# Optimization experiments

Measured on AMD Instinct MI355X. Metric: run time of the kernel, lower is better.

## Reference

```python
import jax, jax.numpy as jnp
import numpy as np

CODEBOOK_SIZE = 8192
EMBED_DIM = 128
BETA = 0.25
TEMPERATURE = 0.1
EPS_NORM = 1e-12  # torch F.normalize eps


def _l2_normalize(x, axis=-1):
    n = jnp.linalg.norm(x, axis=axis, keepdims=True)
    return x / jnp.maximum(n, EPS_NORM)


def setup_inputs() -> dict:
    key = jax.random.key(0)
    kz, kw = jax.random.split(key)
    z = jax.random.normal(kz, (4, 4096, EMBED_DIM), dtype=jnp.float32)
    # torch init is uniform(-1/D, 1/D); normal also exercises the math fine,
    # but stay faithful to scale:
    W = jax.random.uniform(kw, (CODEBOOK_SIZE, EMBED_DIM), dtype=jnp.float32,
                           minval=-1.0 / EMBED_DIM, maxval=1.0 / EMBED_DIM)
    return {"z": z, "W": W}


def reference(z, W):
    orig_shape = z.shape
    z_flat = z.reshape(-1, EMBED_DIM)              # [N, D]
    N = z_flat.shape[0]

    z_norm = _l2_normalize(z_flat, axis=1)
    e_norm = _l2_normalize(W, axis=1)
    scores = z_norm @ e_norm.T                     # [N, K]

    idx = jnp.argmax(scores, axis=1)               # [N]
    z_q = W[idx].reshape(orig_shape)

    counts = jnp.zeros((CODEBOOK_SIZE,), jnp.float32).at[idx].add(1.0)
    e_mean = counts / N
    perplexity = jnp.exp(-jnp.sum(e_mean * jnp.log(e_mean + 1e-8)))

    sg = jax.lax.stop_gradient
    commit_loss = jnp.mean((sg(z_q) - z) ** 2) + BETA * jnp.mean((z_q - sg(z)) ** 2)

    z_q_st = z + sg(z_q - z)                        # straight-through

    log_probs = jax.nn.log_softmax(scores / TEMPERATURE, axis=1)  # [N, K]
    probs = jnp.exp(log_probs)
    P_avg = jnp.mean(probs, axis=0) + 1e-8
    entropy_loss = -jnp.sum(P_avg * jnp.log(P_avg))

    return (z_q_st, commit_loss, perplexity, entropy_loss)
```

## Files before the change

kernel.cpp:

```cpp
#include <hip/hip_runtime.h>
#include <hip/hip_bf16.h>
#include <math.h>

#define N_ROWS 16384
#define DIM 128
#define K_CODES 8192
#define EPS2 2e-3f
#define EPSF 7e-5f

#define OFF_EN       0u
#define OFF_ZN       1048576u
#define OFF_EP       3145728u
#define OFF_ZP       4194304u
#define OFF_ZC       6291456u
#define OFF_PART     7340032u
#define OFF_PART2    7602176u
#define OFF_LINV     7864320u
#define OFF_IDX      7880704u
#define OFF_FLA      7897088u
#define OFF_FLB      7913472u
#define OFF_CNT      7929856u
#define OFF_P        7938048u
#define OFF_MSE      7946240u
#define OFF_NFA      7946241u
#define OFF_NFB      7946242u
#define OFF_REFBUF   7946244u
#define MEMSET_BYTES 196624u

typedef __bf16 bf16x8 __attribute__((ext_vector_type(8)));
typedef float  f32x4  __attribute__((ext_vector_type(4)));
#define MFMA16(a, b, c) __builtin_amdgcn_mfma_f32_16x16x32_bf16(a, b, c, 0, 0, 0)

__device__ __forceinline__ void gld_lds16(const ushort* g, ushort* l) {
    __builtin_amdgcn_global_load_lds(
        (const __attribute__((address_space(1))) unsigned int*)g,
        (__attribute__((address_space(3))) unsigned int*)l, 16, 0, 0);
}

__device__ __forceinline__ ushort f2bf(float x) {
    __hip_bfloat16 b = __float2bfloat16(x);
    return *reinterpret_cast<ushort*>(&b);
}
__device__ __forceinline__ float bf2f(ushort u) {
    __hip_bfloat16 b = *reinterpret_cast<__hip_bfloat16*>(&u);
    return __bfloat162float(b);
}

__device__ __forceinline__ void bf_store2(ushort* __restrict__ P, int T, int r,
                                          int rx, int k, ushort e0, ushort e1) {
    int g = k >> 6, kp = (k >> 3) & 7, j = k & 7;
    int off = (((((T << 2) + g) << 10) + (r << 3) + (kp ^ rx)) << 3) + j;
    *reinterpret_cast<ushort2*>(&P[off]) = make_ushort2(e0, e1);
}

__global__ __launch_bounds__(256) void k_prep(const float* __restrict__ z,
                                              const float* __restrict__ W,
                                              float* __restrict__ zN,
                                              float* __restrict__ eN,
                                              ushort* __restrict__ Zp,
                                              ushort* __restrict__ Ep) {
    int t = threadIdx.x, w = t >> 6, lane = t & 63;
    int row = blockIdx.x * 4 + w;
    const float* src; float* dstN; ushort* dstP;
    if (row < N_ROWS) { src = z; dstN = zN; dstP = Zp; }
    else { row -= N_ROWS; src = W; dstN = eN; dstP = Ep; }
    float2 v = *reinterpret_cast<const float2*>(&src[(size_t)row * DIM + lane * 2]);
    float ss = v.x * v.x + v.y * v.y;
#pragma unroll
    for (int off = 32; off; off >>= 1) ss += __shfl_xor(ss, off);
    float nrm = fmaxf(sqrtf(ss), 1e-12f);
    float a = v.x / nrm, b = v.y / nrm;
    *reinterpret_cast<float2*>(&dstN[(size_t)row * DIM + lane * 2]) = make_float2(a, b);
    ushort ha = f2bf(a), hb = f2bf(b);
    ushort la = f2bf(a - bf2f(ha)), lb = f2bf(b - bf2f(hb));
    int T = row >> 7, r = row & 127, rx = r & 7, d = lane * 2;
    bf_store2(dstP, T, r, rx, d, ha, hb);
    bf_store2(dstP, T, r, rx, 128 + d, la, lb);
}

__global__ __launch_bounds__(256, 2) void k_p1(const ushort* __restrict__ Zp,
                                               const ushort* __restrict__ Ep,
                                               float4* __restrict__ part) {
    __shared__ ushort Bu[2][16384];
    int t = threadIdx.x, lane = t & 63, w = t >> 6;
    int rg = blockIdx.x >> 2, slice = blockIdx.x & 3;
    int wm = w >> 1, wn = w & 1;
    int n15 = lane & 15, quad = lane >> 4;
    int T = rg >> 1, rofs = (rg & 1) << 6;

    bf16x8 af[2][2][2];
#pragma unroll
    for (int ms = 0; ms < 2; ++ms) {
        int r = rofs + wm * 32 + ms * 16 + n15, rx = r & 7;
#pragma unroll
        for (int g = 0; g < 2; ++g)
#pragma unroll
            for (int kl = 0; kl < 2; ++kl)
                af[ms][g][kl] = *reinterpret_cast<const bf16x8*>(
                    &Zp[(((((T << 2) + g) << 10) + (r << 3) + (((kl * 4 + quad)) ^ rx)) << 3)]);
    }

    float sm[8], s2v[8], sl[8];
    unsigned si[8];
#pragma unroll
    for (int s = 0; s < 8; ++s) { sm[s] = -1e30f; s2v[s] = -1e30f; sl[s] = 0.f; si[s] = 0u; }

    {
        const ushort* gb = Ep + (((size_t)(slice * 16) << 2) << 13);
#pragma unroll
        for (int it = 0; it < 8; ++it) {
            int cpos = it * 256 + t;
            gld_lds16(gb + (cpos << 3), &Bu[0][cpos << 3]);
        }
    }
    int bufc = 0;
    for (int ch = 0; ch < 16; ++ch) {
        __syncthreads();
        if (ch < 15) {
            const ushort* gb = Ep + (((size_t)((slice * 16 + ch + 1) << 2)) << 13);
            ushort* dst = Bu[bufc ^ 1];
#pragma unroll
            for (int it = 0; it < 8; ++it) {
                int cpos = it * 256 + t;
                gld_lds16(gb + (cpos << 3), &dst[cpos << 3]);
            }
        }
        const ushort* bsrc = Bu[bufc];
        f32x4 acc[2][4];
#pragma unroll
        for (int i = 0; i < 2; ++i)
#pragma unroll
            for (int j = 0; j < 4; ++j) acc[i][j] = (f32x4)2.0f;
#pragma unroll
        for (int g = 0; g < 2; ++g)
#pragma unroll
            for (int kl = 0; kl < 2; ++kl) {
                bf16x8 bfr[4];
#pragma unroll
                for (int ns = 0; ns < 4; ++ns) {
                    int c = wn * 64 + ns * 16 + n15;
                    int kx = (kl * 4 + quad) ^ (c & 7);
                    bfr[ns] = *reinterpret_cast<const bf16x8*>(
                        &bsrc[(((g << 10) + (c << 3) + kx) << 3)]);
                }
#pragma unroll
                for (int ms = 0; ms < 2; ++ms)
#pragma unroll
                    for (int ns = 0; ns < 4; ++ns)
                        acc[ms][ns] = MFMA16(af[ms][g][kl], bfr[ns], acc[ms][ns]);
            }
        unsigned cbase = (unsigned)((slice * 16 + ch) * 128 + wn * 64 + n15);
#pragma unroll
        for (int ms = 0; ms < 2; ++ms)
#pragma unroll
            for (int reg = 0; reg < 4; ++reg) {
                int s = ms * 4 + reg;
                float m = sm[s], m2 = s2v[s], l = 0.f;
                unsigned idx = si[s];
#pragma unroll
                for (int ns = 0; ns < 4; ++ns) {
                    float v = acc[ms][ns][reg];
                    l += __expf(fmaf(v, 10.f, -20.f));
                    float lo = fminf(v, m);
                    m2 = fmaxf(m2, lo);
                    idx = (v > m) ? (cbase + ns * 16) : idx;
                    m = fmaxf(v, m);
                }
                sl[s] += l; sm[s] = m; s2v[s] = m2; si[s] = idx;
            }
        bufc ^= 1;
    }
#pragma unroll
    for (int ms = 0; ms < 2; ++ms)
#pragma unroll
        for (int reg = 0; reg < 4; ++reg) {
            int s = ms * 4 + reg;
            float m = sm[s], m2 = s2v[s], l = sl[s];
            unsigned idx = si[s];
#pragma unroll
            for (int off = 1; off < 16; off <<= 1) {
                float om  = __shfl_xor(m, off);
                float om2 = __shfl_xor(m2, off);
                float ol  = __shfl_xor(l, off);
                unsigned oi = (unsigned)__shfl_xor((int)idx, off);
                m2 = fmaxf(fmaxf(m2, om2), fminf(m, om));
                l += ol;
                bool take = (om > m) || (om == m && oi < idx);
                idx = take ? oi : idx;
                m = fmaxf(m, om);
            }
            if (n15 == 0) {
                int row = rg * 64 + wm * 32 + ms * 16 + quad * 4 + reg;
                part[slice * N_ROWS + row] = make_float4(m, l, __uint_as_float(idx), m2);
            }
        }
}

__global__ __launch_bounds__(256) void k_merge(const float4* __restrict__ part,
                                               float* __restrict__ linv_out,
                                               int* __restrict__ idx_out,
                                               unsigned int* __restrict__ counts,
                                               int* __restrict__ flaglistA,
                                               int* __restrict__ nfA) {
    int row = blockIdx.x * 256 + threadIdx.x;
    float m = -1e30f, m2 = -1e30f, l = 0.f;
    unsigned idx = 0u;
#pragma unroll
    for (int s = 0; s < 4; ++s) {
        float4 p = part[s * N_ROWS + row];
        float om = p.x, ol = p.y, om2 = p.w;
        unsigned oi = __float_as_uint(p.z);
        m2 = fmaxf(fmaxf(m2, om2), fminf(m, om));
        l += ol;
        bool take = (om > m) || (om == m && oi < idx);
        idx = take ? oi : idx;
        m = fmaxf(m, om);
    }
    linv_out[row] = 1.0f / l;
    idx_out[row] = (int)idx;
    atomicAdd(&counts[idx], 1u);
    if (m - m2 < EPS2) {
        int pos = atomicAdd(nfA, 1);
        if (pos < 8192) flaglistA[pos] = row;
    }
}

__global__ __launch_bounds__(256) void k_gather2(const ushort* __restrict__ Zp,
                                                 const int* __restrict__ flaglistA,
                                                 const int* __restrict__ nfA,
                                                 ushort* __restrict__ Zc) {
    int nf2 = *nfA; if (nf2 > 8192) nf2 = 8192;
    int total = nf2 * 32;
    const uint4* srcv = reinterpret_cast<const uint4*>(Zp);
    uint4* dstv = reinterpret_cast<uint4*>(Zc);
    for (int c = blockIdx.x * 256 + threadIdx.x; c < total; c += 65536) {
        int crow = c >> 5, g = (c >> 3) & 3, kp = c & 7;
        int row = flaglistA[crow];
        int Ts = row >> 7, rs = row & 127;
        int sidx = (((Ts << 2) + g) << 10) + (rs << 3) + (kp ^ (rs & 7));
        int Td = crow >> 6, rd = crow & 63;
        int didx = (((Td << 2) + g) << 9) + (rd << 3) + (kp ^ (rd & 7));
        dstv[didx] = srcv[sidx];
    }
}

__global__ __launch_bounds__(256, 2) void k_s2(const ushort* __restrict__ Zc,
                                               const ushort* __restrict__ Ep,
                                               const int* __restrict__ nfA,
                                               float4* __restrict__ part2) {
    __shared__ ushort Bu[2][8192];
    int nf2 = *nfA; if (nf2 > 8192) nf2 = 8192;
    int cg2 = blockIdx.x >> 3, csl = blockIdx.x & 7;
    if (cg2 * 64 >= nf2) return;
    int t = threadIdx.x, lane = t & 63, w = t >> 6;
    int wm = w >> 1, wn = w & 1;
    int n15 = lane & 15, quad = lane >> 4;

    bf16x8 af[2][4][2];
#pragma unroll
    for (int ms = 0; ms < 2; ++ms) {
        int r = wm * 32 + ms * 16 + n15, rx = r & 7;
#pragma unroll
        for (int gz = 0; gz < 4; ++gz)
#pragma unroll
            for (int kl = 0; kl < 2; ++kl)
                af[ms][gz][kl] = *reinterpret_cast<const bf16x8*>(
                    &Zc[(((((cg2 << 2) + gz) << 9) + (r << 3) + ((kl * 4 + quad) ^ rx)) << 3)]);
    }

    float sm[8], s2v[8];
    unsigned si[8];
#pragma unroll
    for (int s = 0; s < 8; ++s) { sm[s] = -1e30f; s2v[s] = -1e30f; si[s] = 0u; }

    {
        const ushort* gb = Ep + (((size_t)((csl * 8) << 2)) << 13);
#pragma unroll
        for (int it = 0; it < 4; ++it) {
            int cpos = it * 256 + t;
            gld_lds16(gb + (cpos << 3), &Bu[0][cpos << 3]);
        }
    }
    int bufc = 0;
    f32x4 acc[2][4];
#pragma unroll
    for (int i = 0; i < 2; ++i)
#pragma unroll
        for (int j = 0; j < 4; ++j) acc[i][j] = (f32x4)2.0f;

    for (int st = 0; st < 32; ++st) {
        __syncthreads();
        if (st < 31) {
            int nx = st + 1;
            const ushort* gb = Ep + (((size_t)(((csl * 8 + (nx >> 2)) << 2) + (nx & 3))) << 13);
            ushort* dst = Bu[bufc ^ 1];
#pragma unroll
            for (int it = 0; it < 4; ++it) {
                int cpos = it * 256 + t;
                gld_lds16(gb + (cpos << 3), &dst[cpos << 3]);
            }
        }
        const ushort* bsrc = Bu[bufc];
        int ge = st & 3;
        int a0 = ge & 1, a1 = (ge & 1) + 2;
        bool two = (ge < 2);
#pragma unroll
        for (int kl = 0; kl < 2; ++kl) {
            bf16x8 bfr[4];
#pragma unroll
            for (int ns = 0; ns < 4; ++ns) {
                int c = wn * 64 + ns * 16 + n15;
                int kx = (kl * 4 + quad) ^ (c & 7);
                bfr[ns] = *reinterpret_cast<const bf16x8*>(&bsrc[(((c << 3) + kx) << 3)]);
            }
#pragma unroll
            for (int ms = 0; ms < 2; ++ms)
#pragma unroll
                for (int ns = 0; ns < 4; ++ns)
                    acc[ms][ns] = MFMA16(af[ms][a0][kl], bfr[ns], acc[ms][ns]);
            if (two) {
#pragma unroll
                for (int ms = 0; ms < 2; ++ms)
#pragma unroll
                    for (int ns = 0; ns < 4; ++ns)
                        acc[ms][ns] = MFMA16(af[ms][a1][kl], bfr[ns], acc[ms][ns]);
            }
        }
        if (ge == 3) {
            int ch = st >> 2;
            unsigned cbase = (unsigned)((csl * 8 + ch) * 128 + wn * 64 + n15);
#pragma unroll
            for (int ms = 0; ms < 2; ++ms)
#pragma unroll
                for (int reg = 0; reg < 4; ++reg) {
                    int s = ms * 4 + reg;
                    float m = sm[s], m2 = s2v[s];
                    unsigned idx = si[s];
#pragma unroll
                    for (int ns = 0; ns < 4; ++ns) {
                        float v = acc[ms][ns][reg];
                        float lo = fminf(v, m);
                        m2 = fmaxf(m2, lo);
                        idx = (v > m) ? (cbase + ns * 16) : idx;
                        m = fmaxf(v, m);
                    }
                    sm[s] = m; s2v[s] = m2; si[s] = idx;
                }
#pragma unroll
            for (int i = 0; i < 2; ++i)
#pragma unroll
                for (int j = 0; j < 4; ++j) acc[i][j] = (f32x4)2.0f;
        }
        bufc ^= 1;
    }
#pragma unroll
    for (int ms = 0; ms < 2; ++ms)
#pragma unroll
        for (int reg = 0; reg < 4; ++reg) {
            int s = ms * 4 + reg;
            float m = sm[s], m2 = s2v[s];
            unsigned idx = si[s];
#pragma unroll
            for (int off = 1; off < 16; off <<= 1) {
                float om  = __shfl_xor(m, off);
                float om2 = __shfl_xor(m2, off);
                unsigned oi = (unsigned)__shfl_xor((int)idx, off);
                m2 = fmaxf(fmaxf(m2, om2), fminf(m, om));
                bool take = (om > m) || (om == m && oi < idx);
                idx = take ? oi : idx;
                m = fmaxf(m, om);
            }
            if (n15 == 0) {
                int crow = cg2 * 64 + wm * 32 + ms * 16 + quad * 4 + reg;
                part2[csl * 8192 + crow] = make_float4(m, 0.f, __uint_as_float(idx), m2);
            }
        }
}

__global__ __launch_bounds__(256) void k_merge2(const float4* __restrict__ part2,
                                                const int* __restrict__ flaglistA,
                                                const int* __restrict__ nfA,
                                                int* __restrict__ idx_arr,
                                                unsigned int* __restrict__ counts,
                                                int* __restrict__ flaglistB,
                                                int* __restrict__ nfB) {
    int i = blockIdx.x * 256 + threadIdx.x;
    int nf2 = *nfA; if (nf2 > 8192) nf2 = 8192;
    if (i >= nf2) return;
    int row = flaglistA[i];
    float m = -1e30f, m2 = -1e30f;
    unsigned idx = 0u;
#pragma unroll
    for (int s = 0; s < 8; ++s) {
        float4 p = part2[s * 8192 + i];
        float om = p.x, om2 = p.w;
        unsigned oi = __float_as_uint(p.z);
        m2 = fmaxf(fmaxf(m2, om2), fminf(m, om));
        bool take = (om > m) || (om == m && oi < idx);
        idx = take ? oi : idx;
        m = fmaxf(m, om);
    }
    int newi = (int)idx, oldi = idx_arr[row];
    if (newi != oldi) {
        idx_arr[row] = newi;
        atomicAdd(&counts[oldi], 0xFFFFFFFFu);
        atomicAdd(&counts[newi], 1u);
    }
    if (m - m2 < EPSF) {
        int pos = atomicAdd(nfB, 1);
        if (pos < N_ROWS) flaglistB[pos] = row;
    }
}

__global__ __launch_bounds__(256) void k_refine(const float* __restrict__ zN,
                                                const float* __restrict__ eN,
                                                const int* __restrict__ flaglistB,
                                                const int* __restrict__ nfB,
                                                unsigned long long* __restrict__ refbuf) {
    int nf = *nfB;
    if (nf > N_ROWS) nf = N_ROWS;
    int csl = blockIdx.x & 7;
    int t = threadIdx.x;
    __shared__ float zl[DIM];
    for (int fi = blockIdx.x >> 3; fi < nf; fi += 512) {
        int row = flaglistB[fi];
        __syncthreads();
        if (t < DIM) zl[t] = zN[(size_t)row * DIM + t];
        __syncthreads();
        double best = -1e300;
        int bc = 0x7FFFFFFF;
#pragma unroll
        for (int j = 0; j < 4; ++j) {
            int c = csl * 1024 + j * 256 + t;
            const float* e = &eN[(size_t)c * DIM];
            double s = 0.0;
#pragma unroll 8
            for (int d = 0; d < DIM; ++d) s += (double)zl[d] * (double)e[d];
            if (s > best) { best = s; bc = c; }
        }
#pragma unroll
        for (int off = 1; off < 64; off <<= 1) {
            double ob = __shfl_xor(best, off);
            int oc = __shfl_xor(bc, off);
            if (ob > best || (ob == best && oc < bc)) { best = ob; bc = oc; }
        }
        if ((t & 63) == 0) {
            unsigned long long u = (unsigned long long)__double_as_longlong(best);
            u = (u & 0x8000000000000000ull) ? ~u : (u | 0x8000000000000000ull);
            unsigned long long key = (u & ~0x1FFFull) | (unsigned long long)(8191 - bc);
            atomicMax(&refbuf[row], key);
        }
    }
}

__global__ __launch_bounds__(256) void k_fixidx(const int* __restrict__ flaglistB,
                                                const int* __restrict__ nfB,
                                                const unsigned long long* __restrict__ refbuf,
                                                int* __restrict__ idx,
                                                unsigned int* __restrict__ counts) {
    int i = blockIdx.x * 256 + threadIdx.x;
    int nf = *nfB;
    if (nf > N_ROWS) nf = N_ROWS;
    if (i < nf) {
        int row = flaglistB[i];
        int newi = 8191 - (int)(refbuf[row] & 0x1FFFull);
        int oldi = idx[row];
        if (newi != oldi) {
            idx[row] = newi;
            atomicAdd(&counts[oldi], 0xFFFFFFFFu);
            atomicAdd(&counts[newi], 1u);
        }
    }
}

__global__ __launch_bounds__(256, 2) void k_p2(const ushort* __restrict__ Zp,
                                               const ushort* __restrict__ Ep,
                                               const float* __restrict__ linv_in,
                                               float* __restrict__ P_sum) {
    __shared__ ushort Bu[2][16384];
    int t = threadIdx.x, lane = t & 63, w = t >> 6;
    int cg = blockIdx.x >> 2, rslice = blockIdx.x & 3;
    int wm = w >> 1, wn = w & 1;
    int n15 = lane & 15, quad = lane >> 4;
    int T = cg >> 1, cofs = (cg & 1) << 6;

    bf16x8 af[2][2][2];
#pragma unroll
    for (int ms = 0; ms < 2; ++ms) {
        int c = cofs + wm * 32 + ms * 16 + n15, cx = c & 7;
#pragma unroll
        for (int g = 0; g < 2; ++g)
#pragma unroll
            for (int kl = 0; kl < 2; ++kl)
                af[ms][g][kl] = *reinterpret_cast<const bf16x8*>(
                    &Ep[(((((T << 2) + g) << 10) + (c << 3) + ((kl * 4 + quad) ^ cx)) << 3)]);
    }

    float pacc[8];
#pragma unroll
    for (int s = 0; s < 8; ++s) pacc[s] = 0.f;

    {
        const ushort* gb = Zp + (((size_t)((rslice * 32) << 2)) << 13);
#pragma unroll
        for (int it = 0; it < 8; ++it) {
            int cpos = it * 256 + t;
            gld_lds16(gb + (cpos << 3), &Bu[0][cpos << 3]);
        }
    }
    int bufc = 0;
    for (int ch = 0; ch < 32; ++ch) {
        __syncthreads();
        if (ch < 31) {
            const ushort* gb = Zp + (((size_t)((rslice * 32 + ch + 1) << 2)) << 13);
            ushort* dst = Bu[bufc ^ 1];
#pragma unroll
            for (int it = 0; it < 8; ++it) {
                int cpos = it * 256 + t;
                gld_lds16(gb + (cpos << 3), &dst[cpos << 3]);
            }
        }
        const ushort* bsrc = Bu[bufc];
        f32x4 acc[2][4];
#pragma unroll
        for (int i = 0; i < 2; ++i)
#pragma unroll
            for (int j = 0; j < 4; ++j) acc[i][j] = (f32x4)2.0f;
#pragma unroll
        for (int g = 0; g < 2; ++g)
#pragma unroll
            for (int kl = 0; kl < 2; ++kl) {
                bf16x8 bfr[4];
#pragma unroll
                for (int ns = 0; ns < 4; ++ns) {
                    int r = wn * 64 + ns * 16 + n15;
                    int kx = (kl * 4 + quad) ^ (r & 7);
                    bfr[ns] = *reinterpret_cast<const bf16x8*>(
                        &bsrc[(((g << 10) + (r << 3) + kx) << 3)]);
                }
#pragma unroll
                for (int ms = 0; ms < 2; ++ms)
#pragma unroll
                    for (int ns = 0; ns < 4; ++ns)
                        acc[ms][ns] = MFMA16(af[ms][g][kl], bfr[ns], acc[ms][ns]);
            }
        int rbase = (rslice * 32 + ch) * 128 + wn * 64 + n15;
        float li[4];
#pragma unroll
        for (int ns = 0; ns < 4; ++ns) li[ns] = linv_in[rbase + ns * 16];
#pragma unroll
        for (int ms = 0; ms < 2; ++ms)
#pragma unroll
            for (int reg = 0; reg < 4; ++reg) {
                int s = ms * 4 + reg;
                float p = pacc[s];
#pragma unroll
                for (int ns = 0; ns < 4; ++ns)
                    p = fmaf(__expf(fmaf(acc[ms][ns][reg], 10.f, -20.f)), li[ns], p);
                pacc[s] = p;
            }
        bufc ^= 1;
    }
#pragma unroll
    for (int s = 0; s < 8; ++s) {
#pragma unroll
        for (int off = 1; off < 16; off <<= 1) pacc[s] += __shfl_xor(pacc[s], off);
    }
    if (n15 == 0) {
#pragma unroll
        for (int ms = 0; ms < 2; ++ms)
#pragma unroll
            for (int reg = 0; reg < 4; ++reg)
                atomicAdd(&P_sum[cg * 64 + wm * 32 + ms * 16 + quad * 4 + reg],
                          pacc[ms * 4 + reg]);
    }
}

__global__ __launch_bounds__(256) void k_gather(const float* __restrict__ z,
                                                const float* __restrict__ W,
                                                const int* __restrict__ idx,
                                                float* __restrict__ out,
                                                float* __restrict__ mse) {
    int v = blockIdx.x * 256 + threadIdx.x;
    int row = v >> 5;
    int id = idx[row];
    float4 q = *reinterpret_cast<const float4*>(&W[(size_t)id * DIM + (v & 31) * 4]);
    float4 zz = *reinterpret_cast<const float4*>(&z[(size_t)v * 4]);
    float dx = q.x - zz.x, dy = q.y - zz.y, dz = q.z - zz.z, dw = q.w - zz.w;
    *reinterpret_cast<float4*>(&out[(size_t)v * 4]) = q;
    float e = dx * dx + dy * dy + dz * dz + dw * dw;
#pragma unroll
    for (int off = 1; off < 64; off <<= 1) e += __shfl_xor(e, off);
    __shared__ float red[4];
    int lane = threadIdx.x & 63, wv = threadIdx.x >> 6;
    if (lane == 0) red[wv] = e;
    __syncthreads();
    if (threadIdx.x == 0) atomicAdd(mse, red[0] + red[1] + red[2] + red[3]);
}

__global__ __launch_bounds__(256) void k_finalize(const unsigned int* __restrict__ counts,
                                                  const float* __restrict__ P_sum,
                                                  const float* __restrict__ mse,
                                                  float* __restrict__ out) {
    int t = threadIdx.x;
    float s1 = 0.f, s2 = 0.f;
    for (int k = t; k < K_CODES; k += 256) {
        float em = (float)counts[k] * (1.0f / 16384.0f);
        s1 += em * logf(em + 1e-8f);
        float p = P_sum[k] * (1.0f / 16384.0f) + 1e-8f;
        s2 += p * logf(p);
    }
#pragma unroll
    for (int off = 1; off < 64; off <<= 1) {
        s1 += __shfl_xor(s1, off);
        s2 += __shfl_xor(s2, off);
    }
    __shared__ float r1[4], r2[4];
    int lane = t & 63, wv = t >> 6;
    if (lane == 0) { r1[wv] = s1; r2[wv] = s2; }
    __syncthreads();
    if (t == 0) {
        float S1 = r1[0] + r1[1] + r1[2] + r1[3];
        float S2 = r2[0] + r2[1] + r2[2] + r2[3];
        out[2097152] = 1.25f * mse[0] * (1.0f / 2097152.0f);
        out[2097153] = expf(-S1);
        out[2097154] = -S2;
    }
}

extern "C" void kernel_launch(void* const* d_in, const int* in_sizes, int n_in,
                              void* d_out, int out_size, void* d_ws, size_t ws_size,
                              hipStream_t stream) {
    (void)in_sizes; (void)n_in; (void)out_size; (void)ws_size;
    const float* z = (const float*)d_in[0];
    const float* W = (const float*)d_in[1];
    float* ws = (float*)d_ws;
    float* eN = ws + OFF_EN;
    float* zN = ws + OFF_ZN;
    ushort* Ep = (ushort*)(ws + OFF_EP);
    ushort* Zp = (ushort*)(ws + OFF_ZP);
    ushort* Zc = (ushort*)(ws + OFF_ZC);
    float4* part = (float4*)(ws + OFF_PART);
    float4* part2 = (float4*)(ws + OFF_PART2);
    float* linv = ws + OFF_LINV;
    int* idx = (int*)(ws + OFF_IDX);
    int* flaglistA = (int*)(ws + OFF_FLA);
    int* flaglistB = (int*)(ws + OFF_FLB);
    unsigned int* counts = (unsigned int*)(ws + OFF_CNT);
    float* P = ws + OFF_P;
    float* mse = ws + OFF_MSE;
    int* nfA = (int*)(ws + OFF_NFA);
    int* nfB = (int*)(ws + OFF_NFB);
    unsigned long long* refbuf = (unsigned long long*)(ws + OFF_REFBUF);
    float* out = (float*)d_out;

    hipMemsetAsync(ws + OFF_CNT, 0, MEMSET_BYTES, stream);
    k_prep<<<(N_ROWS + K_CODES) / 4, 256, 0, stream>>>(z, W, zN, eN, Zp, Ep);
    k_p1<<<1024, 256, 0, stream>>>(Zp, Ep, part);
    k_merge<<<N_ROWS / 256, 256, 0, stream>>>(part, linv, idx, counts, flaglistA, nfA);
    k_gather2<<<256, 256, 0, stream>>>(Zp, flaglistA, nfA, Zc);
    k_s2<<<1024, 256, 0, stream>>>(Zc, Ep, nfA, part2);
    k_merge2<<<32, 256, 0, stream>>>(part2, flaglistA, nfA, idx, counts, flaglistB, nfB);
    k_refine<<<4096, 256, 0, stream>>>(zN, eN, flaglistB, nfB, refbuf);
    k_fixidx<<<64, 256, 0, stream>>>(flaglistB, nfB, refbuf, idx, counts);
    k_p2<<<512, 256, 0, stream>>>(Zp, Ep, linv, P);
    k_gather<<<(N_ROWS * DIM / 4) / 256, 256, 0, stream>>>(z, W, idx, out, mse);
    k_finalize<<<1, 256, 0, stream>>>(counts, P, mse, out);
}
```

Before: 309.7 us.

## Halve LDS staging tiles, raise occupancy, pack argmax index into score bits

k_p1 and k_p2 now stage 64-column half tiles, so the LDS double buffer is half as large and launch bounds rise to 4 blocks per SM. k_p2 also doubles its grid by splitting the row slices. k_p1 encodes the candidate index in the low 6 mantissa bits of each score, so the running max carries the index and the separate index registers and selects go away. Exponentials use exp2 with pre-scaled constants. The hipMemsetAsync is replaced by zeroing inside k_prep, saving one launch. The mantissa packing slightly perturbs score values, so near-ties may resolve differently, and the smaller tiles double the number of barriers.

```diff
diff --git a/kernel.cpp b/kernel.cpp
--- a/kernel.cpp
+++ b/kernel.cpp
@@ -25,11 +25,22 @@
 #define OFF_NFA      7946241u
 #define OFF_NFB      7946242u
 #define OFF_REFBUF   7946244u
-#define MEMSET_BYTES 196624u
+#define ZERO_WORDS   49156u
 
 typedef __bf16 bf16x8 __attribute__((ext_vector_type(8)));
 typedef float  f32x4  __attribute__((ext_vector_type(4)));
 #define MFMA16(a, b, c) __builtin_amdgcn_mfma_f32_16x16x32_bf16(a, b, c, 0, 0, 0)
+
+#if defined(__has_builtin)
+#if __has_builtin(__builtin_amdgcn_exp2f)
+#define EXP2F(x) __builtin_amdgcn_exp2f(x)
+#endif
+#endif
+#ifndef EXP2F
+#define EXP2F(x) exp2f(x)
+#endif
+#define L2E10 14.4269504089f
+#define L2E10B 28.8539008178f
 
 __device__ __forceinline__ void gld_lds16(const ushort* g, ushort* l) {
     __builtin_amdgcn_global_load_lds(
@@ -53,13 +64,29 @@
     *reinterpret_cast<ushort2*>(&P[off]) = make_ushort2(e0, e1);
 }
 
+__device__ __forceinline__ void stage64(const ushort* __restrict__ src, int Tc, int h,
+                                        ushort* __restrict__ dst, int t) {
+#pragma unroll
+    for (int it = 0; it < 4; ++it) {
+        int i = it * 256 + t;
+        int g = i >> 9, within = i & 511;
+        int schunk = (((Tc << 2) + g) << 10) + (h << 9) + within;
+        gld_lds16(src + ((size_t)schunk << 3), dst + ((size_t)((g << 9) + within) << 3));
+    }
+}
+
 __global__ __launch_bounds__(256) void k_prep(const float* __restrict__ z,
                                               const float* __restrict__ W,
                                               float* __restrict__ zN,
                                               float* __restrict__ eN,
                                               ushort* __restrict__ Zp,
-                                              ushort* __restrict__ Ep) {
+                                              ushort* __restrict__ Ep,
+                                              unsigned* __restrict__ zr) {
     int t = threadIdx.x, w = t >> 6, lane = t & 63;
+    if (blockIdx.x < 193) {
+        unsigned i = blockIdx.x * 256 + t;
+        if (i < ZERO_WORDS) zr[i] = 0u;
+    }
     int row = blockIdx.x * 4 + w;
     const float* src; float* dstN; ushort* dstP;
     if (row < N_ROWS) { src = z; dstN = zN; dstP = Zp; }
@@ -78,10 +105,10 @@
     bf_store2(dstP, T, r, rx, 128 + d, la, lb);
 }
 
-__global__ __launch_bounds__(256, 2) void k_p1(const ushort* __restrict__ Zp,
+__global__ __launch_bounds__(256, 4) void k_p1(const ushort* __restrict__ Zp,
                                                const ushort* __restrict__ Ep,
                                                float4* __restrict__ part) {
-    __shared__ ushort Bu[2][16384];
+    __shared__ ushort Bu[2][8192];
     int t = threadIdx.x, lane = t & 63, w = t >> 6;
     int rg = blockIdx.x >> 2, slice = blockIdx.x & 3;
     int wm = w >> 1, wn = w & 1;
@@ -97,77 +124,79 @@
 #pragma unroll
             for (int kl = 0; kl < 2; ++kl)
                 af[ms][g][kl] = *reinterpret_cast<const bf16x8*>(
-                    &Zp[(((((T << 2) + g) << 10) + (r << 3) + (((kl * 4 + quad)) ^ rx)) << 3)]);
+                    &Zp[(((((T << 2) + g) << 10) + (r << 3) + ((kl * 4 + quad) ^ rx)) << 3)]);
     }
 
     float sm[8], s2v[8], sl[8];
-    unsigned si[8];
-#pragma unroll
-    for (int s = 0; s < 8; ++s) { sm[s] = -1e30f; s2v[s] = -1e30f; sl[s] = 0.f; si[s] = 0u; }
-
-    {
-        const ushort* gb = Ep + (((size_t)(slice * 16) << 2) << 13);
-#pragma unroll
-        for (int it = 0; it < 8; ++it) {
-            int cpos = it * 256 + t;
-            gld_lds16(gb + (cpos << 3), &Bu[0][cpos << 3]);
-        }
-    }
+#pragma unroll
+    for (int s = 0; s < 8; ++s) { sm[s] = -1e30f; s2v[s] = -1e30f; sl[s] = 0.f; }
+
+    stage64(Ep, slice * 16, 0, Bu[0], t);
     int bufc = 0;
-    for (int ch = 0; ch < 16; ++ch) {
+    f32x4 acc[2][4];
+#pragma unroll
+    for (int i = 0; i < 2; ++i)
+#pragma unroll
+        for (int j = 0; j < 4; ++j) acc[i][j] = (f32x4)2.0f;
+
+    for (int st = 0; st < 32; ++st) {
         __syncthreads();
-        if (ch < 15) {
-            const ushort* gb = Ep + (((size_t)((slice * 16 + ch + 1) << 2)) << 13);
-            ushort* dst = Bu[bufc ^ 1];
-#pragma unroll
-            for (int it = 0; it < 8; ++it) {
-                int cpos = it * 256 + t;
-                gld_lds16(gb + (cpos << 3), &dst[cpos << 3]);
-            }
+        if (st < 31) {
+            int nx = st + 1;
+            stage64(Ep, slice * 16 + (nx >> 1), nx & 1, Bu[bufc ^ 1], t);
         }
         const ushort* bsrc = Bu[bufc];
-        f32x4 acc[2][4];
-#pragma unroll
-        for (int i = 0; i < 2; ++i)
-#pragma unroll
-            for (int j = 0; j < 4; ++j) acc[i][j] = (f32x4)2.0f;
+        int sp = st & 1;
 #pragma unroll
         for (int g = 0; g < 2; ++g)
 #pragma unroll
             for (int kl = 0; kl < 2; ++kl) {
-                bf16x8 bfr[4];
-#pragma unroll
-                for (int ns = 0; ns < 4; ++ns) {
-                    int c = wn * 64 + ns * 16 + n15;
+                bf16x8 bfr[2];
+#pragma unroll
+                for (int nsl = 0; nsl < 2; ++nsl) {
+                    int c = wn * 32 + nsl * 16 + n15;
                     int kx = (kl * 4 + quad) ^ (c & 7);
-                    bfr[ns] = *reinterpret_cast<const bf16x8*>(
-                        &bsrc[(((g << 10) + (c << 3) + kx) << 3)]);
+                    bfr[nsl] = *reinterpret_cast<const bf16x8*>(
+                        &bsrc[((size_t)((g << 9) + (c << 3) + kx)) << 3]);
                 }
 #pragma unroll
                 for (int ms = 0; ms < 2; ++ms)
 #pragma unroll
-                    for (int ns = 0; ns < 4; ++ns)
-                        acc[ms][ns] = MFMA16(af[ms][g][kl], bfr[ns], acc[ms][ns]);
-            }
-        unsigned cbase = (unsigned)((slice * 16 + ch) * 128 + wn * 64 + n15);
-#pragma unroll
-        for (int ms = 0; ms < 2; ++ms)
-#pragma unroll
-            for (int reg = 0; reg < 4; ++reg) {
-                int s = ms * 4 + reg;
-                float m = sm[s], m2 = s2v[s], l = 0.f;
-                unsigned idx = si[s];
-#pragma unroll
-                for (int ns = 0; ns < 4; ++ns) {
-                    float v = acc[ms][ns][reg];
-                    l += __expf(fmaf(v, 10.f, -20.f));
-                    float lo = fminf(v, m);
-                    m2 = fmaxf(m2, lo);
-                    idx = (v > m) ? (cbase + ns * 16) : idx;
-                    m = fmaxf(v, m);
+                    for (int nsl = 0; nsl < 2; ++nsl)
+                        acc[ms][sp * 2 + nsl] = MFMA16(af[ms][g][kl], bfr[nsl], acc[ms][sp * 2 + nsl]);
+            }
+        if (sp) {
+            int pair = st >> 1;
+            unsigned base6 = 63u - (unsigned)(pair * 4);
+#pragma unroll
+            for (int ms = 0; ms < 2; ++ms)
+#pragma unroll
+                for (int reg = 0; reg < 4; ++reg) {
+                    int s = ms * 4 + reg;
+                    float v0 = acc[ms][0][reg], v1 = acc[ms][1][reg];
+                    float v2 = acc[ms][2][reg], v3 = acc[ms][3][reg];
+                    float e0 = EXP2F(fmaf(v0, L2E10, -L2E10B));
+                    float e1 = EXP2F(fmaf(v1, L2E10, -L2E10B));
+                    float e2 = EXP2F(fmaf(v2, L2E10, -L2E10B));
+                    float e3 = EXP2F(fmaf(v3, L2E10, -L2E10B));
+                    sl[s] += (e0 + e1) + (e2 + e3);
+                    float f0 = __uint_as_float((__float_as_uint(v0) & 0xFFFFFFC0u) | (base6 - 0u));
+                    float f1 = __uint_as_float((__float_as_uint(v1) & 0xFFFFFFC0u) | (base6 - 1u));
+                    float f2 = __uint_as_float((__float_as_uint(v2) & 0xFFFFFFC0u) | (base6 - 2u));
+                    float f3 = __uint_as_float((__float_as_uint(v3) & 0xFFFFFFC0u) | (base6 - 3u));
+                    float a  = fmaxf(f0, f1), b = fminf(f0, f1);
+                    float c2 = fmaxf(f2, f3), d = fminf(f2, f3);
+                    float chmax = fmaxf(a, c2);
+                    float sec4 = fmaxf(fmaxf(fminf(a, c2), b), d);
+                    float mo = sm[s];
+                    s2v[s] = fmaxf(fmaxf(s2v[s], fminf(mo, chmax)), sec4);
+                    sm[s] = fmaxf(mo, chmax);
                 }
-                sl[s] += l; sm[s] = m; s2v[s] = m2; si[s] = idx;
-            }
+#pragma unroll
+            for (int i = 0; i < 2; ++i)
+#pragma unroll
+                for (int j = 0; j < 4; ++j) acc[i][j] = (f32x4)2.0f;
+        }
         bufc ^= 1;
     }
 #pragma unroll
@@ -176,7 +205,10 @@
         for (int reg = 0; reg < 4; ++reg) {
             int s = ms * 4 + reg;
             float m = sm[s], m2 = s2v[s], l = sl[s];
-            unsigned idx = si[s];
+            unsigned c6 = 63u - (__float_as_uint(m) & 63u);
+            int pair = (int)(c6 >> 2), j = (int)(c6 & 3u);
+            unsigned idx = (unsigned)(slice * 2048 + pair * 128 + wn * 32 +
+                                      (j >> 1) * 64 + (j & 1) * 16 + n15);
 #pragma unroll
             for (int off = 1; off < 16; off <<= 1) {
                 float om  = __shfl_xor(m, off);
@@ -473,13 +505,13 @@
     }
 }
 
-__global__ __launch_bounds__(256, 2) void k_p2(const ushort* __restrict__ Zp,
+__global__ __launch_bounds__(256, 4) void k_p2(const ushort* __restrict__ Zp,
                                                const ushort* __restrict__ Ep,
                                                const float* __restrict__ linv_in,
                                                float* __restrict__ P_sum) {
-    __shared__ ushort Bu[2][16384];
+    __shared__ ushort Bu[2][8192];
     int t = threadIdx.x, lane = t & 63, w = t >> 6;
-    int cg = blockIdx.x >> 2, rslice = blockIdx.x & 3;
+    int cg = blockIdx.x >> 3, rslice = blockIdx.x & 7;
     int wm = w >> 1, wn = w & 1;
     int n15 = lane & 15, quad = lane >> 4;
     int T = cg >> 1, cofs = (cg & 1) << 6;
@@ -500,63 +532,48 @@
 #pragma unroll
     for (int s = 0; s < 8; ++s) pacc[s] = 0.f;
 
-    {
-        const ushort* gb = Zp + (((size_t)((rslice * 32) << 2)) << 13);
-#pragma unroll
-        for (int it = 0; it < 8; ++it) {
-            int cpos = it * 256 + t;
-            gld_lds16(gb + (cpos << 3), &Bu[0][cpos << 3]);
-        }
-    }
+    stage64(Zp, rslice * 16, 0, Bu[0], t);
     int bufc = 0;
-    for (int ch = 0; ch < 32; ++ch) {
+    for (int st = 0; st < 32; ++st) {
         __syncthreads();
-        if (ch < 31) {
-            const ushort* gb = Zp + (((size_t)((rslice * 32 + ch + 1) << 2)) << 13);
-            ushort* dst = Bu[bufc ^ 1];
-#pragma unroll
-            for (int it = 0; it < 8; ++it) {
-                int cpos = it * 256 + t;
-                gld_lds16(gb + (cpos << 3), &dst[cpos << 3]);
-            }
+        if (st < 31) {
+            int nx = st + 1;
+            stage64(Zp, rslice * 16 + (nx >> 1), nx & 1, Bu[bufc ^ 1], t);
         }
         const ushort* bsrc = Bu[bufc];
-        f32x4 acc[2][4];
+        f32x4 acc[2][2];
 #pragma unroll
         for (int i = 0; i < 2; ++i)
 #pragma unroll
-            for (int j = 0; j < 4; ++j) acc[i][j] = (f32x4)2.0f;
+            for (int j = 0; j < 2; ++j) acc[i][j] = (f32x4)2.0f;
 #pragma unroll
         for (int g = 0; g < 2; ++g)
 #pragma unroll
             for (int kl = 0; kl < 2; ++kl) {
-                bf16x8 bfr[4];
-#pragma unroll
-                for (int ns = 0; ns < 4; ++ns) {
-                    int r = wn * 64 + ns * 16 + n15;
+                bf16x8 bfr[2];
+#pragma unroll
+                for (int nsl = 0; nsl < 2; ++nsl) {
+                    int r = wn * 32 + nsl * 16 + n15;
                     int kx = (kl * 4 + quad) ^ (r & 7);
-                    bfr[ns] = *reinterpret_cast<const bf16x8*>(
-                        &bsrc[(((g << 10) + (r << 3) + kx) << 3)]);
+                    bfr[nsl] = *reinterpret_cast<const bf16x8*>(
+                        &bsrc[((size_t)((g << 9) + (r << 3) + kx)) << 3]);
                 }
 #pragma unroll
                 for (int ms = 0; ms < 2; ++ms)
 #pragma unroll
-                    for (int ns = 0; ns < 4; ++ns)
-                        acc[ms][ns] = MFMA16(af[ms][g][kl], bfr[ns], acc[ms][ns]);
-            }
-        int rbase = (rslice * 32 + ch) * 128 + wn * 64 + n15;
-        float li[4];
-#pragma unroll
-        for (int ns = 0; ns < 4; ++ns) li[ns] = linv_in[rbase + ns * 16];
+                    for (int nsl = 0; nsl < 2; ++nsl)
+                        acc[ms][nsl] = MFMA16(af[ms][g][kl], bfr[nsl], acc[ms][nsl]);
+            }
+        int rbase = rslice * 2048 + st * 64 + wn * 32 + n15;
+        float li0 = linv_in[rbase], li1 = linv_in[rbase + 16];
 #pragma unroll
         for (int ms = 0; ms < 2; ++ms)
 #pragma unroll
             for (int reg = 0; reg < 4; ++reg) {
                 int s = ms * 4 + reg;
                 float p = pacc[s];
-#pragma unroll
-                for (int ns = 0; ns < 4; ++ns)
-                    p = fmaf(__expf(fmaf(acc[ms][ns][reg], 10.f, -20.f)), li[ns], p);
+                p = fmaf(EXP2F(fmaf(acc[ms][0][reg], L2E10, -L2E10B)), li0, p);
+                p = fmaf(EXP2F(fmaf(acc[ms][1][reg], L2E10, -L2E10B)), li1, p);
                 pacc[s] = p;
             }
         bufc ^= 1;
@@ -654,8 +671,7 @@
     unsigned long long* refbuf = (unsigned long long*)(ws + OFF_REFBUF);
     float* out = (float*)d_out;
 
-    hipMemsetAsync(ws + OFF_CNT, 0, MEMSET_BYTES, stream);
-    k_prep<<<(N_ROWS + K_CODES) / 4, 256, 0, stream>>>(z, W, zN, eN, Zp, Ep);
+    k_prep<<<(N_ROWS + K_CODES) / 4, 256, 0, stream>>>(z, W, zN, eN, Zp, Ep, counts);
     k_p1<<<1024, 256, 0, stream>>>(Zp, Ep, part);
     k_merge<<<N_ROWS / 256, 256, 0, stream>>>(part, linv, idx, counts, flaglistA, nfA);
     k_gather2<<<256, 256, 0, stream>>>(Zp, flaglistA, nfA, Zc);
@@ -663,7 +679,7 @@
     k_merge2<<<32, 256, 0, stream>>>(part2, flaglistA, nfA, idx, counts, flaglistB, nfB);
     k_refine<<<4096, 256, 0, stream>>>(zN, eN, flaglistB, nfB, refbuf);
     k_fixidx<<<64, 256, 0, stream>>>(flaglistB, nfB, refbuf, idx, counts);
-    k_p2<<<512, 256, 0, stream>>>(Zp, Ep, linv, P);
+    k_p2<<<1024, 256, 0, stream>>>(Zp, Ep, linv, P);
     k_gather<<<(N_ROWS * DIM / 4) / 256, 256, 0, stream>>>(z, W, idx, out, mse);
     k_finalize<<<1, 256, 0, stream>>>(counts, P, mse, out);
 }
```

Result: slower. 500.1 us (+61.5%).
